# Kernel optimization log

Hardware: AMD Instinct MI355X
Metric: run time of the kernel (lower is better)

The kernel has to match this reference:

```python
import jax, jax.numpy as jnp
import numpy as np

N_HEAD = 16
COND_LEN = 256  # n_unmasked; mask[i, j] == 1 iff j < COND_LEN + i


def rotate_half(x):
    # interleaved pairs: (x0, x1, x2, x3, ...) -> (-x1, x0, -x3, x2, ...)
    x = x.reshape(x.shape[:-1] + (-1, 2))
    x1, x2 = x[..., 0], x[..., 1]
    return jnp.stack([-x2, x1], axis=-1).reshape(x.shape[:-2] + (-1,))


def apply_rotary_pos_emb(t, freqs):
    # t: [B, H, T, l], freqs: [T, l] -> broadcast over B, H
    return t * jnp.cos(freqs) + rotate_half(t) * jnp.sin(freqs)


def setup_inputs() -> dict:
    key = jax.random.key(0)
    ks = jax.random.split(key, 12)
    B, T, C = 8, 769, 1024
    l = 32
    s = 0.02
    return {
        "x_q": jax.random.normal(ks[0], (B, T, C), jnp.float32),
        "x_kv": jax.random.normal(ks[1], (B, T, C), jnp.float32),
        "rotary_pos_emb": jax.random.uniform(ks[2], (T, l), jnp.float32),
        "Wq": jax.random.normal(ks[3], (C, C), jnp.float32) * s,
        "bq": jnp.zeros((C,), jnp.float32),
        "Wk": jax.random.normal(ks[4], (C, C), jnp.float32) * s,
        "bk": jnp.zeros((C,), jnp.float32),
        "Wv": jax.random.normal(ks[5], (C, C), jnp.float32) * s,
        "bv": jnp.zeros((C,), jnp.float32),
        "Wp": jax.random.normal(ks[6], (C, C), jnp.float32) * s,
        "bp": jnp.zeros((C,), jnp.float32),
    }


def reference(x_q, x_kv, rotary_pos_emb, Wq, bq, Wk, bk, Wv, bv, Wp, bp):
    B, T_q, C = x_q.shape
    T_kv = x_kv.shape[1]
    H = N_HEAD
    hd = C // H

    def heads(x, W, b, T):
        return (x @ W.T + b).reshape(B, T, H, hd).transpose(0, 2, 1, 3)  # [B,H,T,hd]

    q = heads(x_q, Wq, bq, T_q)
    k = heads(x_kv, Wk, bk, T_kv)
    v = heads(x_kv, Wv, bv, T_kv)

    # partial rotary on first l dims of q and k
    l = rotary_pos_emb.shape[-1]
    q = jnp.concatenate([apply_rotary_pos_emb(q[..., :l], rotary_pos_emb), q[..., l:]], axis=-1)
    k = jnp.concatenate([apply_rotary_pos_emb(k[..., :l], rotary_pos_emb), k[..., l:]], axis=-1)

    att = jnp.einsum("bhqd,bhkd->bhqk", q, k) * (1.0 / jnp.sqrt(jnp.asarray(hd, q.dtype)))
    # custom prefix+causal mask: allowed iff col < COND_LEN + row
    row = jnp.arange(T_q)[:, None]
    col = jnp.arange(T_kv)[None, :]
    allowed = col < (COND_LEN + row)  # [T_q, T_kv]
    att = jnp.where(allowed[None, None], att, -jnp.inf)
    att = jax.nn.softmax(att, axis=-1)

    y = jnp.einsum("bhqk,bhkd->bhqd", att, v)
    y = y.transpose(0, 2, 1, 3).reshape(B, T_q, C)
    return y @ Wp.T + bp
```

## Files before the change

kernel.cpp:

```cpp
#include <hip/hip_runtime.h>
#include <stdint.h>

#define B_    8
#define T_    769
#define C_    1024
#define H_    16
#define COND_ 256
#define NTOK  (B_*T_)
#define BH_   (B_*H_)
#define TP_   896

typedef short    v8s  __attribute__((ext_vector_type(8)));
typedef float    v4f  __attribute__((ext_vector_type(4)));
typedef uint16_t u16x4 __attribute__((ext_vector_type(4)));
typedef uint16_t u16x8 __attribute__((ext_vector_type(8)));

__device__ __forceinline__ uint16_t f2bf(float f) {
  uint32_t u = __builtin_bit_cast(uint32_t, f);
  u += 0x7fffu + ((u >> 16) & 1u);
  return (uint16_t)(u >> 16);
}
__device__ __forceinline__ float bf2f(uint16_t h) {
  uint32_t u = ((uint32_t)h) << 16;
  return __builtin_bit_cast(float, u);
}

__device__ __forceinline__ void gl_lds16(const void* gptr, void* lptr) {
  __builtin_amdgcn_global_load_lds(
      (const __attribute__((address_space(1))) uint32_t*)gptr,
      (__attribute__((address_space(3))) uint32_t*)lptr,
      16, 0, 0);
}

__device__ __forceinline__ int xcd_swz(int bid, int perxcd) {
  return (bid & 7) * perxcd + (bid >> 3);
}

__global__ __launch_bounds__(256) void convert_bf16(
    const float* xq, const float* xkv, const float* wq, const float* wk,
    const float* wv, const float* wp,
    uint16_t* dxq, uint16_t* dxkv, uint16_t* dwq, uint16_t* dwk,
    uint16_t* dwv, uint16_t* dwp)
{
  int bid = blockIdx.x;
  const float* s; uint16_t* d; int base;
  if (bid < 6152)       { s = xq;  d = dxq;  base = bid; }
  else if (bid < 12304) { s = xkv; d = dxkv; base = bid - 6152; }
  else {
    int r = bid - 12304;
    int wsel = r >> 10; base = r & 1023;
    s = (wsel == 0) ? wq : (wsel == 1) ? wk : (wsel == 2) ? wv : wp;
    d = (wsel == 0) ? dwq : (wsel == 1) ? dwk : (wsel == 2) ? dwv : dwp;
  }
  int i = base * 256 + threadIdx.x;
  float4 f = ((const float4*)s)[i];
  u16x4 o;
  o[0] = f2bf(f.x); o[1] = f2bf(f.y); o[2] = f2bf(f.z); o[3] = f2bf(f.w);
  ((u16x4*)d)[i] = o;
}


__device__ __forceinline__ void gemm_stage64(
    const uint16_t* const Aptr[4], const uint16_t* const Bptr[4],
    int k0, uint16_t* sA, uint16_t* sB, int tid)
{
  #pragma unroll
  for (int r = 0; r < 4; r++) {
    gl_lds16(Aptr[r] + k0, sA + (r * 256 + tid) * 8);
    gl_lds16(Bptr[r] + k0, sB + (r * 256 + tid) * 8);
  }
}

__device__ __forceinline__ void gemm_compute64(
    const uint16_t* sAc, const uint16_t* sBc, v4f acc[4][4],
    int rbase, int cbase, int quad, int l15)
{
  #pragma unroll
  for (int s = 0; s < 2; s++) {
    v8s af[4], bfv[4];
    #pragma unroll
    for (int i = 0; i < 4; i++) {
      int m = rbase + i * 16 + l15;
      af[i] = *(const v8s*)(sAc + m * 64 + (((s * 4 + quad) ^ (m & 7)) * 8));
    }
    #pragma unroll
    for (int j = 0; j < 4; j++) {
      int n = cbase + j * 16 + l15;
      bfv[j] = *(const v8s*)(sBc + n * 64 + (((s * 4 + quad) ^ (n & 7)) * 8));
    }
    #pragma unroll
    for (int i = 0; i < 4; i++)
      #pragma unroll
      for (int j = 0; j < 4; j++)
        acc[i][j] = __builtin_amdgcn_mfma_f32_16x16x32_bf16(af[i], bfv[j], acc[i][j], 0, 0, 0);
  }
}

__device__ __forceinline__ void gemm_mainloop64(
    const uint16_t* A, const uint16_t* W, int M, int row0, int col0,
    v4f acc[4][4], uint16_t* sA, uint16_t* sB)
{
  const int tid = threadIdx.x;
  const int lane = tid & 63, w = tid >> 6, quad = lane >> 4, l15 = lane & 15;
  const int rbase = (w >> 1) * 64, cbase = (w & 1) * 64;

  const uint16_t* Aptr[4];
  const uint16_t* Bptr[4];
  #pragma unroll
  for (int r = 0; r < 4; r++) {
    int c = r * 256 + tid;
    int row = c >> 3, qp = c & 7;
    int g = qp ^ (row & 7);
    Aptr[r] = A + (size_t)min(row0 + row, M - 1) * 1024 + g * 8;
    Bptr[r] = W + (size_t)(col0 + row) * 1024 + g * 8;
  }

  #pragma unroll
  for (int i = 0; i < 4; i++)
    #pragma unroll
    for (int j = 0; j < 4; j++) acc[i][j] = (v4f)0.0f;

  uint16_t* sA0 = sA;         uint16_t* sB0 = sB;
  uint16_t* sA1 = sA + 8192;  uint16_t* sB1 = sB + 8192;

  gemm_stage64(Aptr, Bptr, 0,  sA0, sB0, tid);
  gemm_stage64(Aptr, Bptr, 64, sA1, sB1, tid);

  #pragma unroll 1
  for (int t = 0; t < 16; t++) {
    if (t < 15) {
      asm volatile("s_waitcnt vmcnt(8)" ::: "memory");
    } else {
      asm volatile("s_waitcnt vmcnt(0)" ::: "memory");
    }
    __builtin_amdgcn_s_barrier();
    uint16_t* cA = (t & 1) ? sA1 : sA0;
    uint16_t* cB = (t & 1) ? sB1 : sB0;
    gemm_compute64(cA, cB, acc, rbase, cbase, quad, l15);
    __builtin_amdgcn_s_barrier();
    if (t + 2 < 16)
      gemm_stage64(Aptr, Bptr, (t + 2) * 64, cA, cB, tid);
  }
}

__global__ __launch_bounds__(256) void gemm_qkv(
    const uint16_t* xq, const uint16_t* xkv, const uint16_t* Wqkv,
    const float* bq, const float* bk, const float* bv, const float* freqs,
    uint16_t* Q, uint16_t* K, uint16_t* V)
{
  __shared__ uint16_t sA[2 * 128 * 64];
  __shared__ uint16_t sB[2 * 128 * 64];
  const int swz = xcd_swz(blockIdx.x, 147);
  const int ct = swz % 24, rt = swz / 24;
  const int z = ct >> 3;
  const int col0 = ct * 128, row0 = rt * 128;
  const uint16_t* A = (z == 0) ? xq : xkv;
  const float* bias  = (z == 0) ? bq : (z == 1 ? bk : bv);
  uint16_t* dst      = (z == 0) ? Q  : (z == 1 ? K  : V);

  v4f acc[4][4];
  gemm_mainloop64(A, Wqkv, NTOK, row0, col0, acc, sA, sB);

  const int tid = threadIdx.x;
  const int lane = tid & 63, w = tid >> 6, quad = lane >> 4, l15 = lane & 15;
  const int rbase = (w >> 1) * 64, cbase = (w & 1) * 64;
  #pragma unroll
  for (int i = 0; i < 4; i++) {
    #pragma unroll
    for (int reg = 0; reg < 4; reg++) {
      int n = row0 + rbase + i * 16 + quad * 4 + reg;
      bool ok = (n < NTOK);
      int nn = min(n, NTOK - 1);
      int b = nn / T_, t = nn % T_;
      float vj[4];
      #pragma unroll
      for (int j = 0; j < 4; j++)
        vj[j] = acc[i][j][reg] + bias[(col0 + cbase + j * 16 + l15) & 1023];
      if (z < 2) {
        float v0 = vj[0], v1 = vj[1];
        float p0 = __shfl_xor(v0, 1);
        float p1 = __shfl_xor(v1, 1);
        float f0 = freqs[t * 32 + l15];
        float f1 = freqs[t * 32 + 16 + l15];
        float s0, c0, s1, c1;
        __sincosf(f0, &s0, &c0);
        __sincosf(f1, &s1, &c1);
        if (l15 & 1) { vj[0] = v0 * c0 + p0 * s0; vj[1] = v1 * c1 + p1 * s1; }
        else         { vj[0] = v0 * c0 - p0 * s0; vj[1] = v1 * c1 - p1 * s1; }
      }
      if (z == 0) {
        #pragma unroll
        for (int j = 0; j < 4; j++) vj[j] *= 0.125f;
      }
      if (ok) {
        #pragma unroll
        for (int j = 0; j < 4; j++) {
          int col = col0 + cbase + j * 16 + l15;
          int h = (col >> 6) & 15, d = col & 63;
          dst[((size_t)(b * H_ + h) * T_ + t) * 64 + d] = f2bf(vj[j]);
        }
      }
    }
  }
}

__global__ __launch_bounds__(256) void gemm_out(
    const uint16_t* Y, const uint16_t* wp, const float* bp, float* out)
{
  __shared__ uint16_t sA[2 * 128 * 64];
  __shared__ uint16_t sB[2 * 128 * 64];
  const int swz = xcd_swz(blockIdx.x, 49);
  const int ct = swz & 7, rt = swz >> 3;
  const int col0 = ct * 128, row0 = rt * 128;
  v4f acc[4][4];
  gemm_mainloop64(Y, wp, NTOK, row0, col0, acc, sA, sB);

  const int tid = threadIdx.x;
  const int lane = tid & 63, w = tid >> 6, quad = lane >> 4, l15 = lane & 15;
  const int rbase = (w >> 1) * 64, cbase = (w & 1) * 64;
  #pragma unroll
  for (int i = 0; i < 4; i++) {
    #pragma unroll
    for (int reg = 0; reg < 4; reg++) {
      int n = row0 + rbase + i * 16 + quad * 4 + reg;
      if (n < NTOK) {
        #pragma unroll
        for (int j = 0; j < 4; j++) {
          int col = col0 + cbase + j * 16 + l15;
          out[(size_t)n * 1024 + col] = acc[i][j][reg] + bp[col];
        }
      }
    }
  }
}

__global__ __launch_bounds__(256) void transpose_v(const uint16_t* Vb, uint16_t* Vt)
{
  __shared__ uint16_t sT[64 * 64];
  const int tid = threadIdx.x;
  const int t0 = blockIdx.x * 64, bh = blockIdx.y;
  const uint16_t* src = Vb + (size_t)bh * T_ * 64;
  #pragma unroll
  for (int r = 0; r < 2; r++) {
    int task = r * 256 + tid;
    int t = task >> 3, oc = task & 7;
    int gt = min(t0 + t, T_ - 1);
    u16x8 v = *(const u16x8*)(src + (size_t)gt * 64 + oc * 8);
    int p = oc ^ (t & 7) ^ ((t >> 3) & 7);
    *(u16x8*)(sT + t * 64 + p * 8) = v;
  }
  __syncthreads();
  uint16_t* dst = Vt + (size_t)bh * 64 * TP_;
  #pragma unroll
  for (int r = 0; r < 2; r++) {
    int task = r * 256 + tid;
    int o = task & 7, d = task >> 3;
    u16x8 v;
    #pragma unroll
    for (int k = 0; k < 8; k++) {
      int t = o * 8 + k;
      int p = (d >> 3) ^ k ^ o;
      v[k] = sT[t * 64 + p * 8 + (d & 7)];
    }
    *(u16x8*)(dst + (size_t)d * TP_ + t0 + o * 8) = v;
  }
}

__global__ __launch_bounds__(256) void attn(
    const uint16_t* Q, const uint16_t* K, const uint16_t* Vt, uint16_t* Y)
{
  __shared__ uint16_t sK[128 * 64];
  __shared__ uint16_t sVT[64 * 128];
  __shared__ uint16_t sP[4 * 16 * 136];

  const int tid = threadIdx.x;
  const int lane = tid & 63, w = tid >> 6, quad = lane >> 4, l15 = lane & 15;
  const int swz = xcd_swz(blockIdx.x, 208);
  const int qt = swz % 13, bh = swz / 13;
  const int b = bh >> 4, h = bh & 15;
  const int q0 = qt * 64;

  const uint16_t* Qb = Q + (size_t)bh * T_ * 64;
  const uint16_t* Kb = K + (size_t)bh * T_ * 64;
  const uint16_t* Vtb = Vt + (size_t)bh * 64 * TP_;

  const int qr = min(q0 + w * 16 + l15, T_ - 1);
  v8s aq0 = *(const v8s*)(Qb + (size_t)qr * 64 + quad * 8);
  v8s aq1 = *(const v8s*)(Qb + (size_t)qr * 64 + 32 + quad * 8);

  float l_r[4] = {0.f, 0.f, 0.f, 0.f};
  v4f o[4];
  #pragma unroll
  for (int r = 0; r < 4; r++) o[r] = (v4f)0.0f;

  const int kend = min(T_, q0 + 319);
  const int nkt = (kend + 127) >> 7;

  for (int kt = 0; kt < nkt; kt++) {
    const int k0 = kt * 128;
    #pragma unroll
    for (int r = 0; r < 4; r++) {
      int c = r * 256 + tid;
      int key = c >> 3, qp = c & 7;
      int g = qp ^ (key & 7);
      int gk = min(k0 + key, T_ - 1);
      gl_lds16(Kb + (size_t)gk * 64 + g * 8, sK + c * 8);
    }
    #pragma unroll
    for (int r = 0; r < 4; r++) {
      int c = r * 256 + tid;
      int d = c >> 4, p = c & 15;
      int g = (p & 8) | ((p ^ d) & 7);
      gl_lds16(Vtb + (size_t)d * TP_ + k0 + g * 8, sVT + c * 8);
    }
    __syncthreads();

    v4f s[8];
    #pragma unroll
    for (int cb = 0; cb < 8; cb++) {
      int key_l = cb * 16 + l15;
      v8s b0 = *(const v8s*)(sK + (key_l * 8 + ((quad) ^ (key_l & 7))) * 8);
      v8s b1 = *(const v8s*)(sK + (key_l * 8 + ((4 + quad) ^ (key_l & 7))) * 8);
      v4f zz = (v4f)0.0f;
      zz = __builtin_amdgcn_mfma_f32_16x16x32_bf16(aq0, b0, zz, 0, 0, 0);
      zz = __builtin_amdgcn_mfma_f32_16x16x32_bf16(aq1, b1, zz, 0, 0, 0);
      s[cb] = zz;
    }

    uint16_t* pw = sP + w * (16 * 136);
    const int qrow_base = q0 + w * 16 + quad * 4;
    const bool full = (k0 + 128 <= COND_ + q0) && (k0 + 128 <= T_);
    if (full) {
      #pragma unroll
      for (int reg = 0; reg < 4; reg++) {
        float rs = 0.f;
        #pragma unroll
        for (int cb = 0; cb < 8; cb++) {
          float pv = __expf(s[cb][reg]);
          uint16_t pb = f2bf(pv);
          rs += bf2f(pb);
          pw[(quad * 4 + reg) * 136 + cb * 16 + l15] = pb;
        }
        #pragma unroll
        for (int off = 1; off < 16; off <<= 1) rs += __shfl_xor(rs, off);
        l_r[reg] += rs;
      }
    } else {
      #pragma unroll
      for (int reg = 0; reg < 4; reg++) {
        int lim = min(COND_ + qrow_base + reg, T_);
        float rs = 0.f;
        #pragma unroll
        for (int cb = 0; cb < 8; cb++) {
          int key = k0 + cb * 16 + l15;
          float pv = (key < lim) ? __expf(s[cb][reg]) : 0.f;
          uint16_t pb = f2bf(pv);
          rs += bf2f(pb);
          pw[(quad * 4 + reg) * 136 + cb * 16 + l15] = pb;
        }
        #pragma unroll
        for (int off = 1; off < 16; off <<= 1) rs += __shfl_xor(rs, off);
        l_r[reg] += rs;
      }
    }

    #pragma unroll
    for (int ks = 0; ks < 4; ks++) {
      v8s ap = *(const v8s*)(pw + l15 * 136 + ks * 32 + quad * 8);
      #pragma unroll
      for (int cbd = 0; cbd < 4; cbd++) {
        int d = cbd * 16 + l15;
        v8s bv = *(const v8s*)(sVT + d * 128 + (((ks * 4 + quad) ^ (d & 7)) * 8));
        o[cbd] = __builtin_amdgcn_mfma_f32_16x16x32_bf16(ap, bv, o[cbd], 0, 0, 0);
      }
    }
    __syncthreads();
  }

  #pragma unroll
  for (int reg = 0; reg < 4; reg++) {
    int t = q0 + w * 16 + quad * 4 + reg;
    if (t < T_) {
      float inv = 1.0f / l_r[reg];
      #pragma unroll
      for (int cbd = 0; cbd < 4; cbd++) {
        int d = cbd * 16 + l15;
        Y[((size_t)(b * T_ + t)) * C_ + h * 64 + d] = f2bf(o[cbd][reg] * inv);
      }
    }
  }
}

extern "C" void kernel_launch(void* const* d_in, const int* in_sizes, int n_in,
                              void* d_out, int out_size, void* d_ws, size_t ws_size,
                              hipStream_t stream)
{
  const float* x_q   = (const float*)d_in[0];
  const float* x_kv  = (const float*)d_in[1];
  const float* freqs = (const float*)d_in[2];
  const float* Wq = (const float*)d_in[3];
  const float* bq = (const float*)d_in[4];
  const float* Wk = (const float*)d_in[5];
  const float* bk = (const float*)d_in[6];
  const float* Wv = (const float*)d_in[7];
  const float* bv = (const float*)d_in[8];
  const float* Wp = (const float*)d_in[9];
  const float* bp = (const float*)d_in[10];
  float* out = (float*)d_out;

  const size_t SZX = (size_t)NTOK * C_;
  const size_t SZW = (size_t)C_ * C_;
  uint16_t* ws = (uint16_t*)d_ws;
  uint16_t* xq_bf  = ws;
  uint16_t* xkv_bf = xq_bf + SZX;
  uint16_t* wq_bf  = xkv_bf + SZX;
  uint16_t* wk_bf  = wq_bf + SZW;
  uint16_t* wv_bf  = wk_bf + SZW;
  uint16_t* wp_bf  = wv_bf + SZW;
  uint16_t* Qb = wp_bf + SZW;
  uint16_t* Kb = Qb + SZX;
  uint16_t* Vb = Kb + SZX;
  uint16_t* Vt = ws;
  uint16_t* Yb = Vb;

  convert_bf16<<<dim3(16400), 256, 0, stream>>>(
      x_q, x_kv, Wq, Wk, Wv, Wp, xq_bf, xkv_bf, wq_bf, wk_bf, wv_bf, wp_bf);

  gemm_qkv<<<dim3(1176), 256, 0, stream>>>(
      xq_bf, xkv_bf, wq_bf, bq, bk, bv, freqs, Qb, Kb, Vb);

  transpose_v<<<dim3(13, BH_), 256, 0, stream>>>(Vb, Vt);

  attn<<<dim3(1664), 256, 0, stream>>>(Qb, Kb, Vt, Yb);

  gemm_out<<<dim3(392), 256, 0, stream>>>(Yb, wp_bf, bp, out);
}
```

Baseline: 272.4 us.

## Rewrite QKV GEMM with 256x256 tiles, 512 threads, triple-buffered LDS

Replaces the 128x128 QKV projection GEMM with a 256x256-tile kernel using 8 waves, a triple-buffered LDS pipeline with K-step 32, XOR-swizzled LDS layout, and s_setprio around the MFMA bursts. It also swaps the XCD swizzle for a bijective version that handles grid sizes not divisible by 8, and adds lgkmcnt waits to the older mainloop. The larger tile is meant to raise arithmetic intensity and cut global traffic per flop. In exchange the grid drops to 300 workgroups, which can leave CUs underused, and register pressure rises.

```diff
diff --git a/kernel.cpp b/kernel.cpp
--- a/kernel.cpp
+++ b/kernel.cpp
@@ -32,8 +32,11 @@
       16, 0, 0);
 }
 
-__device__ __forceinline__ int xcd_swz(int bid, int perxcd) {
-  return (bid & 7) * perxcd + (bid >> 3);
+__device__ __forceinline__ int xcd_swz_bij(int orig, int nwg) {
+  int q = nwg >> 3, r = nwg & 7;
+  int xcd = orig & 7;
+  int base = (xcd < r) ? xcd * (q + 1) : r * (q + 1) + (xcd - r) * q;
+  return base + (orig >> 3);
 }
 
 __global__ __launch_bounds__(256) void convert_bf16(
@@ -60,6 +63,168 @@
 }
 
 
+__device__ __forceinline__ int swz4(int m, int c) {
+  return c ^ (m & 3) ^ ((m >> 2) & 3);
+}
+
+struct QOff { int a0[4]; int a1[4]; int b[4]; };
+
+template<int VMC, bool STG>
+__device__ __forceinline__ void ktile256(
+    const uint16_t* cA, const uint16_t* cB, uint16_t* nA, uint16_t* nB,
+    int knext,
+    const uint16_t* ga0, const uint16_t* ga1,
+    const uint16_t* gb0, const uint16_t* gb1,
+    int tid, QOff off, v4f (&acc)[8][4])
+{
+  if (STG) {
+    gl_lds16(ga0 + knext, nA + tid * 8);
+    gl_lds16(gb0 + knext, nB + tid * 8);
+  }
+  asm volatile("s_waitcnt vmcnt(%0)" :: "n"(VMC) : "memory");
+  __builtin_amdgcn_s_barrier();
+  asm volatile("" ::: "memory");
+  v8s a[4], b[4];
+  #pragma unroll
+  for (int i = 0; i < 4; i++) a[i] = *(const v8s*)(cA + off.a0[i]);
+  #pragma unroll
+  for (int j = 0; j < 4; j++) b[j] = *(const v8s*)(cB + off.b[j]);
+  __builtin_amdgcn_s_setprio(1);
+  #pragma unroll
+  for (int i = 0; i < 4; i++)
+    #pragma unroll
+    for (int j = 0; j < 4; j++)
+      acc[i][j] = __builtin_amdgcn_mfma_f32_16x16x32_bf16(a[i], b[j], acc[i][j], 0, 0, 0);
+  __builtin_amdgcn_s_setprio(0);
+  if (STG) {
+    gl_lds16(ga1 + knext, nA + 4096 + tid * 8);
+    gl_lds16(gb1 + knext, nB + 4096 + tid * 8);
+  }
+  v8s a2[4];
+  #pragma unroll
+  for (int i = 0; i < 4; i++) a2[i] = *(const v8s*)(cA + off.a1[i]);
+  asm volatile("s_waitcnt lgkmcnt(0)" ::: "memory");
+  __builtin_amdgcn_s_barrier();
+  asm volatile("" ::: "memory");
+  __builtin_amdgcn_s_setprio(1);
+  #pragma unroll
+  for (int i = 0; i < 4; i++)
+    #pragma unroll
+    for (int j = 0; j < 4; j++)
+      acc[4 + i][j] = __builtin_amdgcn_mfma_f32_16x16x32_bf16(a2[i], b[j], acc[4 + i][j], 0, 0, 0);
+  __builtin_amdgcn_s_setprio(0);
+}
+
+__device__ __forceinline__ void stage_tile256(
+    const uint16_t* ga0, const uint16_t* ga1,
+    const uint16_t* gb0, const uint16_t* gb1,
+    int k0, uint16_t* pA, uint16_t* pB, int tid)
+{
+  gl_lds16(ga0 + k0, pA + tid * 8);
+  gl_lds16(gb0 + k0, pB + tid * 8);
+  gl_lds16(ga1 + k0, pA + 4096 + tid * 8);
+  gl_lds16(gb1 + k0, pB + 4096 + tid * 8);
+}
+
+__global__ __launch_bounds__(512, 2) void gemm_qkv(
+    const uint16_t* xq, const uint16_t* xkv, const uint16_t* Wqkv,
+    const float* bq, const float* bk, const float* bv, const float* freqs,
+    uint16_t* Q, uint16_t* K, uint16_t* V)
+{
+  __shared__ uint16_t sA[3][8192];
+  __shared__ uint16_t sB[3][8192];
+
+  const int tid = threadIdx.x;
+  const int lane = tid & 63, wid = tid >> 6, quad = (lane >> 4), l15 = lane & 15;
+  const int wr = wid >> 2, wc = wid & 3;
+
+  const int swz = xcd_swz_bij(blockIdx.x, 300);
+  const int ct = swz % 12, rt = swz / 12;
+  const int z = ct >> 2;
+  const int col0 = ct * 256, row0 = rt * 256;
+  const uint16_t* A = (z == 0) ? xq : xkv;
+  const float* bias  = (z == 0) ? bq : (z == 1 ? bk : bv);
+  uint16_t* dst      = (z == 0) ? Q  : (z == 1 ? K  : V);
+
+  const int ms = tid >> 2, sl = tid & 3;
+  const int c0 = swz4(ms, sl);
+  const uint16_t* ga0 = A + (size_t)min(row0 + ms,       NTOK - 1) * 1024 + c0 * 8;
+  const uint16_t* ga1 = A + (size_t)min(row0 + 128 + ms, NTOK - 1) * 1024 + c0 * 8;
+  const uint16_t* gb0 = Wqkv + (size_t)(col0 + ms) * 1024 + c0 * 8;
+  const uint16_t* gb1 = Wqkv + (size_t)(col0 + 128 + ms) * 1024 + c0 * 8;
+
+  QOff off;
+  #pragma unroll
+  for (int i = 0; i < 4; i++) {
+    int m0 = wr * 128 + i * 16 + l15;
+    int m1 = m0 + 64;
+    off.a0[i] = m0 * 32 + swz4(m0, quad) * 8;
+    off.a1[i] = m1 * 32 + swz4(m1, quad) * 8;
+    int n = wc * 64 + i * 16 + l15;
+    off.b[i] = n * 32 + swz4(n, quad) * 8;
+  }
+
+  v4f acc[8][4];
+  #pragma unroll
+  for (int i = 0; i < 8; i++)
+    #pragma unroll
+    for (int j = 0; j < 4; j++) acc[i][j] = (v4f)0.0f;
+
+  stage_tile256(ga0, ga1, gb0, gb1, 0,  sA[0], sB[0], tid);
+  stage_tile256(ga0, ga1, gb0, gb1, 32, sA[1], sB[1], tid);
+
+  #pragma unroll 1
+  for (int t3 = 0; t3 < 30; t3 += 3) {
+    ktile256<6, true>(sA[0], sB[0], sA[2], sB[2], (t3 + 2) * 32,
+                      ga0, ga1, gb0, gb1, tid, off, acc);
+    ktile256<6, true>(sA[1], sB[1], sA[0], sB[0], (t3 + 3) * 32,
+                      ga0, ga1, gb0, gb1, tid, off, acc);
+    ktile256<6, true>(sA[2], sB[2], sA[1], sB[1], (t3 + 4) * 32,
+                      ga0, ga1, gb0, gb1, tid, off, acc);
+  }
+  ktile256<4, false>(sA[0], sB[0], sA[2], sB[2], 0, ga0, ga1, gb0, gb1, tid, off, acc);
+  ktile256<0, false>(sA[1], sB[1], sA[2], sB[2], 0, ga0, ga1, gb0, gb1, tid, off, acc);
+
+  #pragma unroll
+  for (int fr = 0; fr < 8; fr++) {
+    #pragma unroll
+    for (int reg = 0; reg < 4; reg++) {
+      int n = row0 + wr * 128 + (fr >> 2) * 64 + (fr & 3) * 16 + quad * 4 + reg;
+      bool ok = (n < NTOK);
+      int nn = min(n, NTOK - 1);
+      int b = nn / T_, t = nn % T_;
+      float vj[4];
+      #pragma unroll
+      for (int j = 0; j < 4; j++)
+        vj[j] = acc[fr][j][reg] + bias[(col0 + wc * 64 + j * 16 + l15) & 1023];
+      if (z < 2) {
+        float v0 = vj[0], v1 = vj[1];
+        float p0 = __shfl_xor(v0, 1);
+        float p1 = __shfl_xor(v1, 1);
+        float f0 = freqs[t * 32 + l15];
+        float f1 = freqs[t * 32 + 16 + l15];
+        float s0, c0_, s1, c1;
+        __sincosf(f0, &s0, &c0_);
+        __sincosf(f1, &s1, &c1);
+        if (l15 & 1) { vj[0] = v0 * c0_ + p0 * s0; vj[1] = v1 * c1 + p1 * s1; }
+        else         { vj[0] = v0 * c0_ - p0 * s0; vj[1] = v1 * c1 - p1 * s1; }
+      }
+      if (z == 0) {
+        #pragma unroll
+        for (int j = 0; j < 4; j++) vj[j] *= 0.125f;
+      }
+      if (ok) {
+        #pragma unroll
+        for (int j = 0; j < 4; j++) {
+          int col = col0 + wc * 64 + j * 16 + l15;
+          int h = (col >> 6) & 15, d = col & 63;
+          dst[((size_t)(b * H_ + h) * T_ + t) * 64 + d] = f2bf(vj[j]);
+        }
+      }
+    }
+  }
+}
+
 __device__ __forceinline__ void gemm_stage64(
     const uint16_t* const Aptr[4], const uint16_t* const Bptr[4],
     int k0, uint16_t* sA, uint16_t* sB, int tid)
@@ -134,82 +299,24 @@
       asm volatile("s_waitcnt vmcnt(0)" ::: "memory");
     }
     __builtin_amdgcn_s_barrier();
+    asm volatile("" ::: "memory");
     uint16_t* cA = (t & 1) ? sA1 : sA0;
     uint16_t* cB = (t & 1) ? sB1 : sB0;
     gemm_compute64(cA, cB, acc, rbase, cbase, quad, l15);
+    asm volatile("s_waitcnt lgkmcnt(0)" ::: "memory");
     __builtin_amdgcn_s_barrier();
+    asm volatile("" ::: "memory");
     if (t + 2 < 16)
       gemm_stage64(Aptr, Bptr, (t + 2) * 64, cA, cB, tid);
   }
 }
 
-__global__ __launch_bounds__(256) void gemm_qkv(
-    const uint16_t* xq, const uint16_t* xkv, const uint16_t* Wqkv,
-    const float* bq, const float* bk, const float* bv, const float* freqs,
-    uint16_t* Q, uint16_t* K, uint16_t* V)
+__global__ __launch_bounds__(256) void gemm_out(
+    const uint16_t* Y, const uint16_t* wp, const float* bp, float* out)
 {
   __shared__ uint16_t sA[2 * 128 * 64];
   __shared__ uint16_t sB[2 * 128 * 64];
-  const int swz = xcd_swz(blockIdx.x, 147);
-  const int ct = swz % 24, rt = swz / 24;
-  const int z = ct >> 3;
-  const int col0 = ct * 128, row0 = rt * 128;
-  const uint16_t* A = (z == 0) ? xq : xkv;
-  const float* bias  = (z == 0) ? bq : (z == 1 ? bk : bv);
-  uint16_t* dst      = (z == 0) ? Q  : (z == 1 ? K  : V);
-
-  v4f acc[4][4];
-  gemm_mainloop64(A, Wqkv, NTOK, row0, col0, acc, sA, sB);
-
-  const int tid = threadIdx.x;
-  const int lane = tid & 63, w = tid >> 6, quad = lane >> 4, l15 = lane & 15;
-  const int rbase = (w >> 1) * 64, cbase = (w & 1) * 64;
-  #pragma unroll
-  for (int i = 0; i < 4; i++) {
-    #pragma unroll
-    for (int reg = 0; reg < 4; reg++) {
-      int n = row0 + rbase + i * 16 + quad * 4 + reg;
-      bool ok = (n < NTOK);
-      int nn = min(n, NTOK - 1);
-      int b = nn / T_, t = nn % T_;
-      float vj[4];
-      #pragma unroll
-      for (int j = 0; j < 4; j++)
-        vj[j] = acc[i][j][reg] + bias[(col0 + cbase + j * 16 + l15) & 1023];
-      if (z < 2) {
-        float v0 = vj[0], v1 = vj[1];
-        float p0 = __shfl_xor(v0, 1);
-        float p1 = __shfl_xor(v1, 1);
-        float f0 = freqs[t * 32 + l15];
-        float f1 = freqs[t * 32 + 16 + l15];
-        float s0, c0, s1, c1;
-        __sincosf(f0, &s0, &c0);
-        __sincosf(f1, &s1, &c1);
-        if (l15 & 1) { vj[0] = v0 * c0 + p0 * s0; vj[1] = v1 * c1 + p1 * s1; }
-        else         { vj[0] = v0 * c0 - p0 * s0; vj[1] = v1 * c1 - p1 * s1; }
-      }
-      if (z == 0) {
-        #pragma unroll
-        for (int j = 0; j < 4; j++) vj[j] *= 0.125f;
-      }
-      if (ok) {
-        #pragma unroll
-        for (int j = 0; j < 4; j++) {
-          int col = col0 + cbase + j * 16 + l15;
-          int h = (col >> 6) & 15, d = col & 63;
-          dst[((size_t)(b * H_ + h) * T_ + t) * 64 + d] = f2bf(vj[j]);
-        }
-      }
-    }
-  }
-}
-
-__global__ __launch_bounds__(256) void gemm_out(
-    const uint16_t* Y, const uint16_t* wp, const float* bp, float* out)
-{
-  __shared__ uint16_t sA[2 * 128 * 64];
-  __shared__ uint16_t sB[2 * 128 * 64];
-  const int swz = xcd_swz(blockIdx.x, 49);
+  const int swz = xcd_swz_bij(blockIdx.x, 392);
   const int ct = swz & 7, rt = swz >> 3;
   const int col0 = ct * 128, row0 = rt * 128;
   v4f acc[4][4];
@@ -275,7 +382,7 @@
 
   const int tid = threadIdx.x;
   const int lane = tid & 63, w = tid >> 6, quad = lane >> 4, l15 = lane & 15;
-  const int swz = xcd_swz(blockIdx.x, 208);
+  const int swz = xcd_swz_bij(blockIdx.x, 1664);
   const int qt = swz % 13, bh = swz / 13;
   const int b = bh >> 4, h = bh & 15;
   const int q0 = qt * 64;
@@ -426,7 +533,7 @@
   convert_bf16<<<dim3(16400), 256, 0, stream>>>(
       x_q, x_kv, Wq, Wk, Wv, Wp, xq_bf, xkv_bf, wq_bf, wk_bf, wv_bf, wp_bf);
 
-  gemm_qkv<<<dim3(1176), 256, 0, stream>>>(
+  gemm_qkv<<<dim3(300), 512, 0, stream>>>(
       xq_bf, xkv_bf, wq_bf, bq, bk, bv, freqs, Qb, Kb, Vb);
 
   transpose_v<<<dim3(13, BH_), 256, 0, stream>>>(Vb, Vt);
```

New measurement: 281.6 us. 1.03x slower.

## Software-pipeline K/V loads in attention and use bijective XCD swizzle

Applied to the files above, without the earlier changes.

Restructures the attention key loop so the next tile's K loads are issued after QK^T finishes and the V loads after PV finishes, overlapping global-to-LDS transfers with compute instead of reloading both behind a full __syncthreads. Replaces the XCD swizzle with a bijective mapping that handles grid sizes not divisible by 8, and adds explicit lgkmcnt waits and compiler barriers around the GEMM mainloop barriers. The split waits on vmcnt counts rely on the exact number of outstanding loads per thread, which is fragile if the staging code changes.

```diff
diff --git a/kernel.cpp b/kernel.cpp
--- a/kernel.cpp
+++ b/kernel.cpp
@@ -32,8 +32,11 @@
       16, 0, 0);
 }
 
-__device__ __forceinline__ int xcd_swz(int bid, int perxcd) {
-  return (bid & 7) * perxcd + (bid >> 3);
+__device__ __forceinline__ int xcd_swz_bij(int orig, int nwg) {
+  int q = nwg >> 3, r = nwg & 7;
+  int xcd = orig & 7;
+  int base = (xcd < r) ? xcd * (q + 1) : r * (q + 1) + (xcd - r) * q;
+  return base + (orig >> 3);
 }
 
 __global__ __launch_bounds__(256) void convert_bf16(
@@ -134,10 +137,13 @@
       asm volatile("s_waitcnt vmcnt(0)" ::: "memory");
     }
     __builtin_amdgcn_s_barrier();
+    asm volatile("" ::: "memory");
     uint16_t* cA = (t & 1) ? sA1 : sA0;
     uint16_t* cB = (t & 1) ? sB1 : sB0;
     gemm_compute64(cA, cB, acc, rbase, cbase, quad, l15);
+    asm volatile("s_waitcnt lgkmcnt(0)" ::: "memory");
     __builtin_amdgcn_s_barrier();
+    asm volatile("" ::: "memory");
     if (t + 2 < 16)
       gemm_stage64(Aptr, Bptr, (t + 2) * 64, cA, cB, tid);
   }
@@ -150,7 +156,7 @@
 {
   __shared__ uint16_t sA[2 * 128 * 64];
   __shared__ uint16_t sB[2 * 128 * 64];
-  const int swz = xcd_swz(blockIdx.x, 147);
+  const int swz = xcd_swz_bij(blockIdx.x, 1176);
   const int ct = swz % 24, rt = swz / 24;
   const int z = ct >> 3;
   const int col0 = ct * 128, row0 = rt * 128;
@@ -209,7 +215,7 @@
 {
   __shared__ uint16_t sA[2 * 128 * 64];
   __shared__ uint16_t sB[2 * 128 * 64];
-  const int swz = xcd_swz(blockIdx.x, 49);
+  const int swz = xcd_swz_bij(blockIdx.x, 392);
   const int ct = swz & 7, rt = swz >> 3;
   const int col0 = ct * 128, row0 = rt * 128;
   v4f acc[4][4];
@@ -275,7 +281,7 @@
 
   const int tid = threadIdx.x;
   const int lane = tid & 63, w = tid >> 6, quad = lane >> 4, l15 = lane & 15;
-  const int swz = xcd_swz(blockIdx.x, 208);
+  const int swz = xcd_swz_bij(blockIdx.x, 1664);
   const int qt = swz % 13, bh = swz / 13;
   const int b = bh >> 4, h = bh & 15;
   const int q0 = qt * 64;
@@ -296,24 +302,36 @@
   const int kend = min(T_, q0 + 319);
   const int nkt = (kend + 127) >> 7;
 
+  #define STAGE_K(K0)                                                     \
+    {                                                                     \
+      _Pragma("unroll")                                                   \
+      for (int r = 0; r < 4; r++) {                                       \
+        int c = r * 256 + tid;                                            \
+        int key = c >> 3, qp = c & 7;                                     \
+        int g = qp ^ (key & 7);                                           \
+        int gk = min((K0) + key, T_ - 1);                                 \
+        gl_lds16(Kb + (size_t)gk * 64 + g * 8, sK + c * 8);               \
+      }                                                                   \
+    }
+  #define STAGE_V(K0)                                                     \
+    {                                                                     \
+      _Pragma("unroll")                                                   \
+      for (int r = 0; r < 4; r++) {                                       \
+        int c = r * 256 + tid;                                            \
+        int d = c >> 4, p = c & 15;                                       \
+        int g = (p & 8) | ((p ^ d) & 7);                                  \
+        gl_lds16(Vtb + (size_t)d * TP_ + (K0) + g * 8, sVT + c * 8);      \
+      }                                                                   \
+    }
+
+  STAGE_K(0);
+  STAGE_V(0);
+
   for (int kt = 0; kt < nkt; kt++) {
     const int k0 = kt * 128;
-    #pragma unroll
-    for (int r = 0; r < 4; r++) {
-      int c = r * 256 + tid;
-      int key = c >> 3, qp = c & 7;
-      int g = qp ^ (key & 7);
-      int gk = min(k0 + key, T_ - 1);
-      gl_lds16(Kb + (size_t)gk * 64 + g * 8, sK + c * 8);
-    }
-    #pragma unroll
-    for (int r = 0; r < 4; r++) {
-      int c = r * 256 + tid;
-      int d = c >> 4, p = c & 15;
-      int g = (p & 8) | ((p ^ d) & 7);
-      gl_lds16(Vtb + (size_t)d * TP_ + k0 + g * 8, sVT + c * 8);
-    }
-    __syncthreads();
+    asm volatile("s_waitcnt vmcnt(4)" ::: "memory");
+    __builtin_amdgcn_s_barrier();
+    asm volatile("" ::: "memory");
 
     v4f s[8];
     #pragma unroll
@@ -364,6 +382,11 @@
       }
     }
 
+    asm volatile("s_waitcnt vmcnt(0)" ::: "memory");
+    __builtin_amdgcn_s_barrier();
+    asm volatile("" ::: "memory");
+    if (kt + 1 < nkt) STAGE_K(k0 + 128);
+
     #pragma unroll
     for (int ks = 0; ks < 4; ks++) {
       v8s ap = *(const v8s*)(pw + l15 * 136 + ks * 32 + quad * 8);
@@ -374,8 +397,14 @@
         o[cbd] = __builtin_amdgcn_mfma_f32_16x16x32_bf16(ap, bv, o[cbd], 0, 0, 0);
       }
     }
-    __syncthreads();
-  }
+
+    asm volatile("s_waitcnt lgkmcnt(0)" ::: "memory");
+    __builtin_amdgcn_s_barrier();
+    asm volatile("" ::: "memory");
+    if (kt + 1 < nkt) STAGE_V(k0 + 128);
+  }
+  #undef STAGE_K
+  #undef STAGE_V
 
   #pragma unroll
   for (int reg = 0; reg < 4; reg++) {
```

After: 274.5 us. No clear change (+0.8%).

## Restructure QKV GEMM to BK=32 with loads-before-barrier and generalize XCD swizzle

Applied to the files above, without the earlier changes.

The QKV projection GEMM now uses a K-step of 32 instead of 64, halving LDS per stage, and uses a new swizzled LDS layout that packs two rows per 64-element line. Each iteration reads its MFMA fragments from LDS before the second barrier, issues the next global-to-LDS prefetch, then runs the MFMAs, so the copy overlaps compute. The XCD block-swizzle helper is replaced with a bijective version that also handles workgroup counts not divisible by 8, and is applied to all three kernels. The output GEMM keeps its old mainloop but gains explicit lgkmcnt waits. The trade-off is twice as many barriers and loop iterations in the QKV GEMM.

```diff
diff --git a/kernel.cpp b/kernel.cpp
--- a/kernel.cpp
+++ b/kernel.cpp
@@ -32,8 +32,11 @@
       16, 0, 0);
 }
 
-__device__ __forceinline__ int xcd_swz(int bid, int perxcd) {
-  return (bid & 7) * perxcd + (bid >> 3);
+__device__ __forceinline__ int xcd_swz_bij(int orig, int nwg) {
+  int q = nwg >> 3, r = nwg & 7;
+  int xcd = orig & 7;
+  int base = (xcd < r) ? xcd * (q + 1) : r * (q + 1) + (xcd - r) * q;
+  return base + (orig >> 3);
 }
 
 __global__ __launch_bounds__(256) void convert_bf16(
@@ -60,97 +63,19 @@
 }
 
 
-__device__ __forceinline__ void gemm_stage64(
-    const uint16_t* const Aptr[4], const uint16_t* const Bptr[4],
-    int k0, uint16_t* sA, uint16_t* sB, int tid)
-{
-  #pragma unroll
-  for (int r = 0; r < 4; r++) {
-    gl_lds16(Aptr[r] + k0, sA + (r * 256 + tid) * 8);
-    gl_lds16(Bptr[r] + k0, sB + (r * 256 + tid) * 8);
-  }
-}
-
-__device__ __forceinline__ void gemm_compute64(
-    const uint16_t* sAc, const uint16_t* sBc, v4f acc[4][4],
-    int rbase, int cbase, int quad, int l15)
-{
-  #pragma unroll
-  for (int s = 0; s < 2; s++) {
-    v8s af[4], bfv[4];
-    #pragma unroll
-    for (int i = 0; i < 4; i++) {
-      int m = rbase + i * 16 + l15;
-      af[i] = *(const v8s*)(sAc + m * 64 + (((s * 4 + quad) ^ (m & 7)) * 8));
-    }
-    #pragma unroll
-    for (int j = 0; j < 4; j++) {
-      int n = cbase + j * 16 + l15;
-      bfv[j] = *(const v8s*)(sBc + n * 64 + (((s * 4 + quad) ^ (n & 7)) * 8));
-    }
-    #pragma unroll
-    for (int i = 0; i < 4; i++)
-      #pragma unroll
-      for (int j = 0; j < 4; j++)
-        acc[i][j] = __builtin_amdgcn_mfma_f32_16x16x32_bf16(af[i], bfv[j], acc[i][j], 0, 0, 0);
-  }
-}
-
-__device__ __forceinline__ void gemm_mainloop64(
-    const uint16_t* A, const uint16_t* W, int M, int row0, int col0,
-    v4f acc[4][4], uint16_t* sA, uint16_t* sB)
-{
-  const int tid = threadIdx.x;
-  const int lane = tid & 63, w = tid >> 6, quad = lane >> 4, l15 = lane & 15;
-  const int rbase = (w >> 1) * 64, cbase = (w & 1) * 64;
-
-  const uint16_t* Aptr[4];
-  const uint16_t* Bptr[4];
-  #pragma unroll
-  for (int r = 0; r < 4; r++) {
-    int c = r * 256 + tid;
-    int row = c >> 3, qp = c & 7;
-    int g = qp ^ (row & 7);
-    Aptr[r] = A + (size_t)min(row0 + row, M - 1) * 1024 + g * 8;
-    Bptr[r] = W + (size_t)(col0 + row) * 1024 + g * 8;
-  }
-
-  #pragma unroll
-  for (int i = 0; i < 4; i++)
-    #pragma unroll
-    for (int j = 0; j < 4; j++) acc[i][j] = (v4f)0.0f;
-
-  uint16_t* sA0 = sA;         uint16_t* sB0 = sB;
-  uint16_t* sA1 = sA + 8192;  uint16_t* sB1 = sB + 8192;
-
-  gemm_stage64(Aptr, Bptr, 0,  sA0, sB0, tid);
-  gemm_stage64(Aptr, Bptr, 64, sA1, sB1, tid);
-
-  #pragma unroll 1
-  for (int t = 0; t < 16; t++) {
-    if (t < 15) {
-      asm volatile("s_waitcnt vmcnt(8)" ::: "memory");
-    } else {
-      asm volatile("s_waitcnt vmcnt(0)" ::: "memory");
-    }
-    __builtin_amdgcn_s_barrier();
-    uint16_t* cA = (t & 1) ? sA1 : sA0;
-    uint16_t* cB = (t & 1) ? sB1 : sB0;
-    gemm_compute64(cA, cB, acc, rbase, cbase, quad, l15);
-    __builtin_amdgcn_s_barrier();
-    if (t + 2 < 16)
-      gemm_stage64(Aptr, Bptr, (t + 2) * 64, cA, cB, tid);
-  }
-}
-
 __global__ __launch_bounds__(256) void gemm_qkv(
     const uint16_t* xq, const uint16_t* xkv, const uint16_t* Wqkv,
     const float* bq, const float* bk, const float* bv, const float* freqs,
     uint16_t* Q, uint16_t* K, uint16_t* V)
 {
-  __shared__ uint16_t sA[2 * 128 * 64];
-  __shared__ uint16_t sB[2 * 128 * 64];
-  const int swz = xcd_swz(blockIdx.x, 147);
+  __shared__ uint16_t sA[2][4096];
+  __shared__ uint16_t sB[2][4096];
+
+  const int tid = threadIdx.x;
+  const int lane = tid & 63, w = tid >> 6, quad = lane >> 4, l15 = lane & 15;
+  const int rbase = (w >> 1) * 64, cbase = (w & 1) * 64;
+
+  const int swz = xcd_swz_bij(blockIdx.x, 1176);
   const int ct = swz % 24, rt = swz / 24;
   const int z = ct >> 3;
   const int col0 = ct * 128, row0 = rt * 128;
@@ -158,12 +83,81 @@
   const float* bias  = (z == 0) ? bq : (z == 1 ? bk : bv);
   uint16_t* dst      = (z == 0) ? Q  : (z == 1 ? K  : V);
 
+  const uint16_t* Ap[2];
+  const uint16_t* Bp[2];
+  #pragma unroll
+  for (int r = 0; r < 2; r++) {
+    int Cc = r * 256 + tid;
+    int sr = Cc >> 3, sc = (Cc & 7) ^ (sr & 7);
+    int row = sr * 2 + (sc >> 2), kc = sc & 3;
+    Ap[r] = A    + (size_t)min(row0 + row, NTOK - 1) * 1024 + kc * 8;
+    Bp[r] = Wqkv + (size_t)(col0 + row) * 1024 + kc * 8;
+  }
+
+  int offA[4], offB[4];
+  #pragma unroll
+  for (int i = 0; i < 4; i++) {
+    int m = rbase + i * 16 + l15;
+    int s0 = m >> 1;
+    offA[i] = s0 * 64 + (((((m & 1) << 2) | quad) ^ (s0 & 7)) * 8);
+    int n = cbase + i * 16 + l15;
+    int sn = n >> 1;
+    offB[i] = sn * 64 + (((((n & 1) << 2) | quad) ^ (sn & 7)) * 8);
+  }
+
   v4f acc[4][4];
-  gemm_mainloop64(A, Wqkv, NTOK, row0, col0, acc, sA, sB);
-
-  const int tid = threadIdx.x;
-  const int lane = tid & 63, w = tid >> 6, quad = lane >> 4, l15 = lane & 15;
-  const int rbase = (w >> 1) * 64, cbase = (w & 1) * 64;
+  #pragma unroll
+  for (int i = 0; i < 4; i++)
+    #pragma unroll
+    for (int j = 0; j < 4; j++) acc[i][j] = (v4f)0.0f;
+
+  #pragma unroll
+  for (int r = 0; r < 2; r++) {
+    gl_lds16(Ap[r] + 0,  sA[0] + (r * 256 + tid) * 8);
+    gl_lds16(Bp[r] + 0,  sB[0] + (r * 256 + tid) * 8);
+  }
+  #pragma unroll
+  for (int r = 0; r < 2; r++) {
+    gl_lds16(Ap[r] + 32, sA[1] + (r * 256 + tid) * 8);
+    gl_lds16(Bp[r] + 32, sB[1] + (r * 256 + tid) * 8);
+  }
+
+  #pragma unroll 1
+  for (int t = 0; t < 32; t++) {
+    if (t < 31) {
+      asm volatile("s_waitcnt vmcnt(4)" ::: "memory");
+    } else {
+      asm volatile("s_waitcnt vmcnt(0)" ::: "memory");
+    }
+    __builtin_amdgcn_s_barrier();
+    asm volatile("" ::: "memory");
+    const uint16_t* cA = (t & 1) ? sA[1] : sA[0];
+    const uint16_t* cB = (t & 1) ? sB[1] : sB[0];
+    v8s af[4], bf[4];
+    #pragma unroll
+    for (int i = 0; i < 4; i++) af[i] = *(const v8s*)(cA + offA[i]);
+    #pragma unroll
+    for (int j = 0; j < 4; j++) bf[j] = *(const v8s*)(cB + offB[j]);
+    asm volatile("s_waitcnt lgkmcnt(0)" ::: "memory");
+    __builtin_amdgcn_s_barrier();
+    asm volatile("" ::: "memory");
+    if (t + 2 < 32) {
+      uint16_t* nA = (t & 1) ? sA[1] : sA[0];
+      uint16_t* nB = (t & 1) ? sB[1] : sB[0];
+      int k0 = (t + 2) * 32;
+      #pragma unroll
+      for (int r = 0; r < 2; r++) {
+        gl_lds16(Ap[r] + k0, nA + (r * 256 + tid) * 8);
+        gl_lds16(Bp[r] + k0, nB + (r * 256 + tid) * 8);
+      }
+    }
+    #pragma unroll
+    for (int i = 0; i < 4; i++)
+      #pragma unroll
+      for (int j = 0; j < 4; j++)
+        acc[i][j] = __builtin_amdgcn_mfma_f32_16x16x32_bf16(af[i], bf[j], acc[i][j], 0, 0, 0);
+  }
+
   #pragma unroll
   for (int i = 0; i < 4; i++) {
     #pragma unroll
@@ -204,12 +198,98 @@
   }
 }
 
+__device__ __forceinline__ void gemm_stage64(
+    const uint16_t* const Aptr[4], const uint16_t* const Bptr[4],
+    int k0, uint16_t* sA, uint16_t* sB, int tid)
+{
+  #pragma unroll
+  for (int r = 0; r < 4; r++) {
+    gl_lds16(Aptr[r] + k0, sA + (r * 256 + tid) * 8);
+    gl_lds16(Bptr[r] + k0, sB + (r * 256 + tid) * 8);
+  }
+}
+
+__device__ __forceinline__ void gemm_compute64(
+    const uint16_t* sAc, const uint16_t* sBc, v4f acc[4][4],
+    int rbase, int cbase, int quad, int l15)
+{
+  #pragma unroll
+  for (int s = 0; s < 2; s++) {
+    v8s af[4], bfv[4];
+    #pragma unroll
+    for (int i = 0; i < 4; i++) {
+      int m = rbase + i * 16 + l15;
+      af[i] = *(const v8s*)(sAc + m * 64 + (((s * 4 + quad) ^ (m & 7)) * 8));
+    }
+    #pragma unroll
+    for (int j = 0; j < 4; j++) {
+      int n = cbase + j * 16 + l15;
+      bfv[j] = *(const v8s*)(sBc + n * 64 + (((s * 4 + quad) ^ (n & 7)) * 8));
+    }
+    #pragma unroll
+    for (int i = 0; i < 4; i++)
+      #pragma unroll
+      for (int j = 0; j < 4; j++)
+        acc[i][j] = __builtin_amdgcn_mfma_f32_16x16x32_bf16(af[i], bfv[j], acc[i][j], 0, 0, 0);
+  }
+}
+
+__device__ __forceinline__ void gemm_mainloop64(
+    const uint16_t* A, const uint16_t* W, int M, int row0, int col0,
+    v4f acc[4][4], uint16_t* sA, uint16_t* sB)
+{
+  const int tid = threadIdx.x;
+  const int lane = tid & 63, w = tid >> 6, quad = lane >> 4, l15 = lane & 15;
+  const int rbase = (w >> 1) * 64, cbase = (w & 1) * 64;
+
+  const uint16_t* Aptr[4];
+  const uint16_t* Bptr[4];
+  #pragma unroll
+  for (int r = 0; r < 4; r++) {
+    int c = r * 256 + tid;
+    int row = c >> 3, qp = c & 7;
+    int g = qp ^ (row & 7);
+    Aptr[r] = A + (size_t)min(row0 + row, M - 1) * 1024 + g * 8;
+    Bptr[r] = W + (size_t)(col0 + row) * 1024 + g * 8;
+  }
+
+  #pragma unroll
+  for (int i = 0; i < 4; i++)
+    #pragma unroll
+    for (int j = 0; j < 4; j++) acc[i][j] = (v4f)0.0f;
+
+  uint16_t* sA0 = sA;         uint16_t* sB0 = sB;
+  uint16_t* sA1 = sA + 8192;  uint16_t* sB1 = sB + 8192;
+
+  gemm_stage64(Aptr, Bptr, 0,  sA0, sB0, tid);
+  gemm_stage64(Aptr, Bptr, 64, sA1, sB1, tid);
+
+  #pragma unroll 1
+  for (int t = 0; t < 16; t++) {
+    if (t < 15) {
+      asm volatile("s_waitcnt vmcnt(8)" ::: "memory");
+    } else {
+      asm volatile("s_waitcnt vmcnt(0)" ::: "memory");
+    }
+    __builtin_amdgcn_s_barrier();
+    asm volatile("" ::: "memory");
+    uint16_t* cA = (t & 1) ? sA1 : sA0;
+    uint16_t* cB = (t & 1) ? sB1 : sB0;
+    gemm_compute64(cA, cB, acc, rbase, cbase, quad, l15);
+    asm volatile("s_waitcnt lgkmcnt(0)" ::: "memory");
+    __builtin_amdgcn_s_barrier();
+    asm volatile("" ::: "memory");
+    if (t + 2 < 16)
+      gemm_stage64(Aptr, Bptr, (t + 2) * 64, cA, cB, tid);
+  }
+}
+
 __global__ __launch_bounds__(256) void gemm_out(
     const uint16_t* Y, const uint16_t* wp, const float* bp, float* out)
 {
   __shared__ uint16_t sA[2 * 128 * 64];
   __shared__ uint16_t sB[2 * 128 * 64];
-  const int swz = xcd_swz(blockIdx.x, 49);
+  const int swz = xcd_swz_bij(blockIdx.x, 392);
   const int ct = swz & 7, rt = swz >> 3;
   const int col0 = ct * 128, row0 = rt * 128;
   v4f acc[4][4];
@@ -275,7 +355,7 @@
 
   const int tid = threadIdx.x;
   const int lane = tid & 63, w = tid >> 6, quad = lane >> 4, l15 = lane & 15;
-  const int swz = xcd_swz(blockIdx.x, 208);
+  const int swz = xcd_swz_bij(blockIdx.x, 1664);
   const int qt = swz % 13, bh = swz / 13;
   const int b = bh >> 4, h = bh & 15;
   const int q0 = qt * 64;
```

After: 267.1 us. About the same (-1.9%).
